# Performance work log

Measured on AMD Instinct MI355X. Metric: run time of the kernel, lower is better.

The kernel has to match this reference:

```python
import jax, jax.numpy as jnp
import numpy as np

N = 50000      # nodes
E = 1000000    # edges (avg degree 20)
IN, H, OUT = 3, 128, 3


def setup_inputs() -> dict:
    key = jax.random.key(0)
    ks = jax.random.split(key, 12)
    pos = jax.random.normal(ks[0], (N, IN), dtype=jnp.float32)
    edge_index = jax.random.randint(ks[1], (2, E), 0, N, dtype=jnp.int64)
    dims = [(IN, H), (H, H), (H, H), (H, H), (H, OUT)]
    inp = {"pos": pos, "edge_index": edge_index}
    for i, (di, do) in enumerate(dims):
        inp[f"W{i}"] = jax.random.normal(ks[2 + 2 * i], (di, do), dtype=jnp.float32) / np.sqrt(di).astype(np.float32)
        inp[f"b{i}"] = jnp.zeros((do,), dtype=jnp.float32)
    return inp


def _gcn_conv(x, W, b, src, dst, norm):
    # PyG GCNConv: linear transform first, then normalized scatter-add, then bias
    h = x @ W                                  # [N, do]
    msg = h[src] * norm[:, None]               # gather + edge-normalize  [E+N, do]
    out = jax.ops.segment_sum(msg, dst, num_segments=N)  # scatter-add to targets
    return out + b


def reference(pos, edge_index, W0, b0, W1, b1, W2, b2, W3, b3, W4, b4):
    src, dst = edge_index[0], edge_index[1]
    loop = jnp.arange(N, dtype=src.dtype)
    src = jnp.concatenate([src, loop])         # add self-loops
    dst = jnp.concatenate([dst, loop])
    # symmetric normalization: deg computed on target nodes incl. self-loops
    deg = jax.ops.segment_sum(jnp.ones_like(src, dtype=pos.dtype), dst, num_segments=N)
    dis = jnp.where(deg > 0, jax.lax.rsqrt(jnp.maximum(deg, 1e-12)), 0.0)
    norm = dis[src] * dis[dst]                 # [E+N]

    Ws = [W0, W1, W2, W3, W4]
    bs = [b0, b1, b2, b3, b4]
    x = pos
    for i in range(4):                         # all but last layer: conv + SiLU
        x = jax.nn.silu(_gcn_conv(x, Ws[i], bs[i], src, dst, norm))
    return _gcn_conv(x, Ws[4], bs[4], src, dst, norm)
```

## Files before the change

kernel.cpp:

```cpp
#include <hip/hip_runtime.h>
#include <cstdint>
#include <cstddef>


#define NB_SPLIT 256
#define BUCKET_SHIFT 7
#define BSLACK 512

static __device__ __forceinline__ float silu_f(float x) {
  return x / (1.0f + __expf(-x));
}

__global__ __launch_bounds__(256) void k_prep(
    const int* __restrict__ e32, int* __restrict__ epack, int* __restrict__ bT,
    int E, int nbucket, int chunk) {
  __shared__ int hist[512];
  __shared__ int nz;
  const int w = blockIdx.x, t = threadIdx.x;
  for (int b = t; b < nbucket; b += 256) hist[b] = 0;
  if (t == 0) nz = 0;
  __syncthreads();
  if (e32[t * 2 + 1] != 0) nz = 1;
  __syncthreads();
  const int f = nz ? 0 : 1;
  const int i0 = w * chunk;
  const int i1 = min(E, i0 + chunk);
  for (int i = i0 + t; i < i1; i += 256) {
    int s, d;
    if (f) { s = e32[2 * i]; d = e32[2 * E + 2 * i]; }
    else   { s = e32[i];     d = e32[E + i]; }
    epack[i] = s | (d << 16);
    atomicAdd(&hist[d >> BUCKET_SHIFT], 1);
  }
  __syncthreads();
  for (int b = t; b < nbucket; b += 256) {
    int h = hist[b];
    if (h) atomicAdd(&bT[b], h);
  }
}

__global__ __launch_bounds__(512) void k_sscan2(
    int* __restrict__ arr, int* __restrict__ cpy, int n) {
  __shared__ int wsum[8];
  const int t = threadIdx.x;
  int v = (t < n) ? arr[t] : 0;
  int sc = v;
  const int lane = t & 63;
  #pragma unroll
  for (int o = 1; o < 64; o <<= 1) {
    int u = __shfl_up(sc, o);
    if (lane >= o) sc += u;
  }
  if (lane == 63) wsum[t >> 6] = sc;
  __syncthreads();
  int wb = 0;
  const int wid = t >> 6;
  for (int w = 0; w < wid; ++w) wb += wsum[w];
  const int ex = wb + sc - v;
  if (t < n) { arr[t] = ex; cpy[t] = ex; }
  if (t == n - 1) arr[n] = ex + v;
}

__global__ __launch_bounds__(256) void k_split(
    const int* __restrict__ epack, int* __restrict__ gcur,
    int* __restrict__ tmp, int E, int nbucket, int chunk) {
  __shared__ int cur[512];
  const int w = blockIdx.x, t = threadIdx.x;
  for (int b = t; b < nbucket; b += 256) cur[b] = 0;
  __syncthreads();
  const int i0 = w * chunk;
  const int i1 = min(E, i0 + chunk);
  for (int i = i0 + t; i < i1; i += 256) {
    int b = (int)(((unsigned)epack[i]) >> (16 + BUCKET_SHIFT));
    atomicAdd(&cur[b], 1);
  }
  __syncthreads();
  for (int b = t; b < nbucket; b += 256) {
    int h = cur[b];
    cur[b] = h ? atomicAdd(&gcur[b], h) : 0;
  }
  __syncthreads();
  for (int i = i0 + t; i < i1; i += 256) {
    int p = epack[i];
    int b = (int)(((unsigned)p) >> (16 + BUCKET_SHIFT));
    int pos = atomicAdd(&cur[b], 1);
    tmp[pos] = p;
  }
}

__global__ __launch_bounds__(256) void k_csr(
    const int* __restrict__ tmp, const int* __restrict__ bbase,
    const float* __restrict__ pos,
    int2* __restrict__ rp, float* __restrict__ dis, float4* __restrict__ p4,
    unsigned short* __restrict__ col, int nbucket, int N) {
  __shared__ int lcnt[128];
  __shared__ int lcur[128];
  __shared__ int wtot;
  const int b = blockIdx.x, t = threadIdx.x;
  const int nb0 = b << BUCKET_SHIFT;
  const int nn = min(1 << BUCKET_SHIFT, N - nb0);
  if (t < 128) lcnt[t] = 0;
  __syncthreads();
  const int s0 = bbase[b], s1 = bbase[b + 1];
  for (int i = s0 + t; i < s1; i += 256) {
    atomicAdd(&lcnt[((unsigned)tmp[i] >> 16) & 127u], 1);
  }
  __syncthreads();
  const int cbase = ((s0 + 3) & ~3) + b * BSLACK;
  int v = 0, pv = 0, sc = 0;
  if (t < 128) {
    v = lcnt[t];
    pv = (v + 3) & ~3;
    sc = pv;
    #pragma unroll
    for (int o = 1; o < 64; o <<= 1) {
      int u = __shfl_up(sc, o);
      if ((t & 63) >= o) sc += u;
    }
    if (t == 63) wtot = sc;
  }
  __syncthreads();
  if (t < 128) {
    int ex = cbase + ((t >= 64) ? wtot : 0) + sc - pv;
    lcur[t] = ex;
    if (t < nn) {
      int node = nb0 + t;
      float d = rsqrtf((float)(v + 1));
      rp[node] = make_int2(ex, pv);
      dis[node] = d;
      p4[node] = make_float4(pos[3 * node + 0] * d, pos[3 * node + 1] * d,
                             pos[3 * node + 2] * d, d);
      for (int p = ex + v; p < ex + pv; ++p) col[p] = (unsigned short)N;
    }
  }
  __syncthreads();
  for (int i = s0 + t; i < s1; i += 256) {
    unsigned p = (unsigned)tmp[i];
    int j = (int)((p >> 16) & ((1u << BUCKET_SHIFT) - 1));
    int pos_ = atomicAdd(&lcur[j], 1);
    col[pos_] = (unsigned short)(p & 0xffffu);
  }
}

__global__ __launch_bounds__(256) void k_l0(
    const float4* __restrict__ p4, const int2* __restrict__ rp,
    const unsigned short* __restrict__ col,
    const float* __restrict__ W0, const float* __restrict__ b0,
    float* __restrict__ out, float* __restrict__ zB, int n, int slStride) {
  const int t = threadIdx.x;
  if (blockIdx.x == 0) {
    const int bi = t >> 7, si = (t >> 4) & 7, ci = t & 15;
    float* bp = bi ? zB : out;
    bp[(size_t)si * slStride + (size_t)n * 16 + ci] = 0.f;
  }
  const int l = t & 31;
  const int node = blockIdx.x * 8 + (t >> 5);
  if (node >= n) return;
  const int2 r = rp[node];
  float a0 = 0.f, a1 = 0.f, a2 = 0.f;
  for (int e = r.x + l; e < r.x + r.y; e += 32) {
    int s = col[e];
    if (s < n) {
      float4 v = p4[s];
      a0 += v.x; a1 += v.y; a2 += v.z;
    }
  }
  #pragma unroll
  for (int m = 16; m >= 1; m >>= 1) {
    a0 += __shfl_xor(a0, m);
    a1 += __shfl_xor(a1, m);
    a2 += __shfl_xor(a2, m);
  }
  const float4 self = p4[node];
  const float d = self.w;
  a0 = (a0 + self.x) * d;
  a1 = (a1 + self.y) * d;
  a2 = (a2 + self.z) * d;
  const int c = l << 2;
  float4 bb = *reinterpret_cast<const float4*>(b0 + c);
  float4 w0 = *reinterpret_cast<const float4*>(W0 + 0 * 128 + c);
  float4 w1 = *reinterpret_cast<const float4*>(W0 + 1 * 128 + c);
  float4 w2 = *reinterpret_cast<const float4*>(W0 + 2 * 128 + c);
  float4 o;
  o.x = silu_f(a0 * w0.x + a1 * w1.x + a2 * w2.x + bb.x) * d;
  o.y = silu_f(a0 * w0.y + a1 * w1.y + a2 * w2.y + bb.y) * d;
  o.z = silu_f(a0 * w0.z + a1 * w1.z + a2 * w2.z + bb.z) * d;
  o.w = silu_f(a0 * w0.w + a1 * w1.w + a2 * w2.w + bb.w) * d;
  *reinterpret_cast<float4*>(out + (size_t)(c >> 4) * slStride +
                             (size_t)node * 16 + (c & 15)) = o;
}

__global__ void k_agg4(const float4* __restrict__ y4, float* __restrict__ out3,
                       const int2* __restrict__ rp,
                       const unsigned short* __restrict__ col,
                       const float* __restrict__ dis, const float* __restrict__ bias,
                       int n) {
  int i = blockIdx.x * blockDim.x + threadIdx.x;
  if (i >= n) return;
  const float4 self = y4[i];
  float a0 = self.x, a1 = self.y, a2 = self.z;
  const int2 r = rp[i];
  for (int e = r.x; e < r.x + r.y; ++e) {
    int s = col[e];
    if (s >= n) continue;
    float4 v = y4[s];
    a0 += v.x; a1 += v.y; a2 += v.z;
  }
  const float d = dis[i];
  out3[i * 3 + 0] = a0 * d + bias[0];
  out3[i * 3 + 1] = a1 * d + bias[1];
  out3[i * 3 + 2] = a2 * d + bias[2];
}

__global__ __launch_bounds__(256) void k_agg_slice(
    const float* __restrict__ xs, float* __restrict__ y,
    const int2* __restrict__ rp, const unsigned short* __restrict__ col,
    const float* __restrict__ dis, int n, int slStride) {
  const int s = blockIdx.x & 7;
  const int nb = blockIdx.x >> 3;
  const int t = threadIdx.x;
  const int lane = t & 63;
  const int nsub = lane >> 3;
  const int ch = (lane >> 2) & 1;
  const int c4 = (lane & 3) << 2;
  const int node = nb * 32 + (t >> 6) * 8 + nsub;
  const bool valid = node < n;
  int e0 = 0, P = 0;
  if (valid) { int2 r = rp[node]; e0 = r.x; P = r.y; }
  const int h = ((P >> 1) + 3) & ~3;
  const int eb = e0 + (ch ? h : 0);
  const int ee = ch ? (e0 + P) : (e0 + h);
  const float* __restrict__ xb = xs + (size_t)s * slStride + c4;

  float4 a0 = make_float4(0.f, 0.f, 0.f, 0.f);
  float4 a1 = make_float4(0.f, 0.f, 0.f, 0.f);
  float4 a2 = make_float4(0.f, 0.f, 0.f, 0.f);
  float4 a3 = make_float4(0.f, 0.f, 0.f, 0.f);
  for (int e = eb; e < ee; e += 4) {
    ushort4 idx = *reinterpret_cast<const ushort4*>(col + e);
    float4 v0 = *reinterpret_cast<const float4*>(xb + (size_t)idx.x * 16);
    float4 v1 = *reinterpret_cast<const float4*>(xb + (size_t)idx.y * 16);
    float4 v2 = *reinterpret_cast<const float4*>(xb + (size_t)idx.z * 16);
    float4 v3 = *reinterpret_cast<const float4*>(xb + (size_t)idx.w * 16);
    a0.x += v0.x; a0.y += v0.y; a0.z += v0.z; a0.w += v0.w;
    a1.x += v1.x; a1.y += v1.y; a1.z += v1.z; a1.w += v1.w;
    a2.x += v2.x; a2.y += v2.y; a2.z += v2.z; a2.w += v2.w;
    a3.x += v3.x; a3.y += v3.y; a3.z += v3.z; a3.w += v3.w;
  }
  a0.x += a1.x + a2.x + a3.x;
  a0.y += a1.y + a2.y + a3.y;
  a0.z += a1.z + a2.z + a3.z;
  a0.w += a1.w + a2.w + a3.w;
  a0.x += __shfl_xor(a0.x, 4);
  a0.y += __shfl_xor(a0.y, 4);
  a0.z += __shfl_xor(a0.z, 4);
  a0.w += __shfl_xor(a0.w, 4);
  if (valid && ch == 0) {
    float4 self = *reinterpret_cast<const float4*>(xb + (size_t)node * 16);
    const float d = dis[node];
    float4 r;
    r.x = (a0.x + self.x) * d;
    r.y = (a0.y + self.y) * d;
    r.z = (a0.z + self.z) * d;
    r.w = (a0.w + self.w) * d;
    *reinterpret_cast<float4*>(y + (size_t)s * slStride + (size_t)node * 16 + c4) = r;
  }
}

template <int PROJ>
__global__ __launch_bounds__(512, 4) void k_mm_w(
    const float* __restrict__ x, const float* __restrict__ W,
    const float* __restrict__ bias, const float* __restrict__ dis,
    float* __restrict__ out, const float* __restrict__ W4, int n, int slStride) {
  __shared__ float ws[128][128];
  const int t = threadIdx.x;
  #pragma unroll
  for (int it = 0; it < 8; ++it) {
    int i = t + it * 512;
    int k = i >> 5, b = i & 31;
    int slot = (b >> 1) | ((b & 1) << 4);
    *reinterpret_cast<float4*>(&ws[k][slot << 2]) =
        *reinterpret_cast<const float4*>(W + (size_t)i * 4);
  }
  __syncthreads();

  const int tc = t & 15;
  const int tr = (t >> 4) << 2;
  const int row0 = blockIdx.x * 128;

  int rb[4];
  #pragma unroll
  for (int r = 0; r < 4; ++r) {
    rb[r] = min(row0 + tr + r, n - 1) * 16;
  }

  float4 accA[4], accB[4];
  #pragma unroll
  for (int r = 0; r < 4; ++r) {
    accA[r] = make_float4(0.f, 0.f, 0.f, 0.f);
    accB[r] = make_float4(0.f, 0.f, 0.f, 0.f);
  }

  #pragma unroll 1
  for (int kk = 0; kk < 128; kk += 4) {
    const float* __restrict__ xk = x + (size_t)(kk >> 4) * slStride + (kk & 15);
    float4 xr[4];
    #pragma unroll
    for (int r = 0; r < 4; ++r) {
      xr[r] = *reinterpret_cast<const float4*>(xk + rb[r]);
    }
    #pragma unroll
    for (int j = 0; j < 4; ++j) {
      float4 wA = *reinterpret_cast<const float4*>(&ws[kk + j][tc << 2]);
      float4 wB = *reinterpret_cast<const float4*>(&ws[kk + j][64 + (tc << 2)]);
      #pragma unroll
      for (int r = 0; r < 4; ++r) {
        float xv = (j == 0) ? xr[r].x : (j == 1) ? xr[r].y : (j == 2) ? xr[r].z : xr[r].w;
        accA[r].x += xv * wA.x; accA[r].y += xv * wA.y;
        accA[r].z += xv * wA.z; accA[r].w += xv * wA.w;
        accB[r].x += xv * wB.x; accB[r].y += xv * wB.y;
        accB[r].z += xv * wB.z; accB[r].w += xv * wB.w;
      }
    }
  }

  float4 bbA = *reinterpret_cast<const float4*>(bias + tc * 8);
  float4 bbB = *reinterpret_cast<const float4*>(bias + tc * 8 + 4);
  if (PROJ) {
    float w4r[8][3];
    #pragma unroll
    for (int c = 0; c < 8; ++c) {
      w4r[c][0] = W4[(tc * 8 + c) * 3 + 0];
      w4r[c][1] = W4[(tc * 8 + c) * 3 + 1];
      w4r[c][2] = W4[(tc * 8 + c) * 3 + 2];
    }
    #pragma unroll
    for (int r = 0; r < 4; ++r) {
      int row = row0 + tr + r;
      float d = (row < n) ? dis[row] : 0.0f;
      float4 a = accA[r], b4 = accB[r];
      a.x = silu_f(a.x + bbA.x) * d;  a.y = silu_f(a.y + bbA.y) * d;
      a.z = silu_f(a.z + bbA.z) * d;  a.w = silu_f(a.w + bbA.w) * d;
      b4.x = silu_f(b4.x + bbB.x) * d; b4.y = silu_f(b4.y + bbB.y) * d;
      b4.z = silu_f(b4.z + bbB.z) * d; b4.w = silu_f(b4.w + bbB.w) * d;
      float p0 = a.x * w4r[0][0] + a.y * w4r[1][0] + a.z * w4r[2][0] + a.w * w4r[3][0]
               + b4.x * w4r[4][0] + b4.y * w4r[5][0] + b4.z * w4r[6][0] + b4.w * w4r[7][0];
      float p1 = a.x * w4r[0][1] + a.y * w4r[1][1] + a.z * w4r[2][1] + a.w * w4r[3][1]
               + b4.x * w4r[4][1] + b4.y * w4r[5][1] + b4.z * w4r[6][1] + b4.w * w4r[7][1];
      float p2 = a.x * w4r[0][2] + a.y * w4r[1][2] + a.z * w4r[2][2] + a.w * w4r[3][2]
               + b4.x * w4r[4][2] + b4.y * w4r[5][2] + b4.z * w4r[6][2] + b4.w * w4r[7][2];
      #pragma unroll
      for (int m = 8; m >= 1; m >>= 1) {
        p0 += __shfl_xor(p0, m);
        p1 += __shfl_xor(p1, m);
        p2 += __shfl_xor(p2, m);
      }
      if ((t & 15) == 0 && row < n) {
        *reinterpret_cast<float4*>(out + (size_t)row * 4) =
            make_float4(p0, p1, p2, 0.f);
      }
    }
  } else {
    #pragma unroll
    for (int r = 0; r < 4; ++r) {
      int row = row0 + tr + r;
      if (row < n) {
        float d = dis[row];
        float4 a = accA[r], b4 = accB[r];
        a.x = silu_f(a.x + bbA.x) * d;  a.y = silu_f(a.y + bbA.y) * d;
        a.z = silu_f(a.z + bbA.z) * d;  a.w = silu_f(a.w + bbA.w) * d;
        b4.x = silu_f(b4.x + bbB.x) * d; b4.y = silu_f(b4.y + bbB.y) * d;
        b4.z = silu_f(b4.z + bbB.z) * d; b4.w = silu_f(b4.w + bbB.w) * d;
        float* dst = out + (size_t)(tc >> 1) * slStride +
                     (size_t)row * 16 + ((tc & 1) << 3);
        *reinterpret_cast<float4*>(dst) = a;
        *reinterpret_cast<float4*>(dst + 4) = b4;
      }
    }
  }
}

extern "C" void kernel_launch(void* const* d_in, const int* in_sizes, int n_in,
                              void* d_out, int out_size, void* d_ws, size_t ws_size,
                              hipStream_t stream) {
  const float* pos = (const float*)d_in[0];
  const int* e32 = (const int*)d_in[1];
  const float* W[5] = {(const float*)d_in[2], (const float*)d_in[4], (const float*)d_in[6],
                       (const float*)d_in[8], (const float*)d_in[10]};
  const float* B[5] = {(const float*)d_in[3], (const float*)d_in[5], (const float*)d_in[7],
                       (const float*)d_in[9], (const float*)d_in[11]};
  float* out = (float*)d_out;

  const int N = in_sizes[0] / 3;
  const int E = in_sizes[1] / 2;
  const int NBUCKET = (N + (1 << BUCKET_SHIFT) - 1) >> BUCKET_SHIFT;
  const int chunk = (E + NB_SPLIT - 1) / NB_SPLIT;
  const int slStride = (N + 1) * 16;

  char* base = (char*)d_ws;
  size_t off = 0;
  auto alloc = [&](size_t bytes) -> void* {
    void* p = base + off;
    off += (bytes + 255) & ~(size_t)255;
    return p;
  };
  float* dis   = (float*)alloc((size_t)N * 4);
  int2* rp     = (int2*)alloc((size_t)N * 8);
  int* bT      = (int*)alloc((size_t)(NBUCKET + 1) * 4);
  int* gcur    = (int*)alloc((size_t)NBUCKET * 4);
  unsigned short* col =
      (unsigned short*)alloc(((size_t)E + (size_t)NBUCKET * BSLACK + 64) * 2);
  float4* p4   = (float4*)alloc((size_t)N * 16);
  float4* y4   = (float4*)alloc((size_t)N * 16);
  float* bufA  = (float*)alloc((size_t)(N + 1) * 128 * 4);
  float* bufB  = (float*)alloc((size_t)(N + 1) * 128 * 4);
  int* epack = (int*)bufA;
  int* tmp   = (int*)bufB;

  hipMemsetAsync(bT, 0, (size_t)(NBUCKET + 1) * 4, stream);
  k_prep<<<NB_SPLIT, 256, 0, stream>>>(e32, epack, bT, E, NBUCKET, chunk);
  k_sscan2<<<1, 512, 0, stream>>>(bT, gcur, NBUCKET);
  k_split<<<NB_SPLIT, 256, 0, stream>>>(epack, gcur, tmp, E, NBUCKET, chunk);
  k_csr<<<NBUCKET, 256, 0, stream>>>(tmp, bT, pos, rp, dis, p4, col, NBUCKET, N);

  k_l0<<<(N + 7) / 8, 256, 0, stream>>>(p4, rp, col, W[0], B[0], bufA, bufB, N, slStride);

  const int agg_grid = ((N + 31) / 32) * 8;
  const int mm_grid = (N + 127) / 128;
  for (int l = 1; l <= 2; ++l) {
    k_agg_slice<<<agg_grid, 256, 0, stream>>>(bufA, bufB, rp, col, dis, N, slStride);
    k_mm_w<0><<<mm_grid, 512, 0, stream>>>(bufB, W[l], B[l], dis, bufA, nullptr, N, slStride);
  }

  k_agg_slice<<<agg_grid, 256, 0, stream>>>(bufA, bufB, rp, col, dis, N, slStride);
  k_mm_w<1><<<mm_grid, 512, 0, stream>>>(bufB, W[3], B[3], dis, (float*)y4, W[4], N, slStride);

  k_agg4<<<(N + 255) / 256, 256, 0, stream>>>(y4, out, rp, col, dis, B[4], N);

  (void)n_in; (void)out_size; (void)ws_size;
}
```

Measured before the change: 310.6 us.

## Fuse CSR histogram and split using fixed per-bucket regions; nontemporal gathers

The edge-preprocessing pipeline (histogram, global scan, split) collapses into one fused split kernel. Each bucket now gets a fixed-size region of BREG slots instead of exact prefix-summed offsets, which removes the scan kernel, the memset, and the second pass over the packed edge array. Packed edges are held in registers between the count and scatter phases. Aggregation gathers switch to nontemporal vector loads. The risk is silent overflow if any bucket receives more than 4096 edges (expected about 2560 for random inputs), plus more memory for col; the nontemporal hint may hurt cache reuse of gathered rows.

```diff
diff --git a/kernel.cpp b/kernel.cpp
--- a/kernel.cpp
+++ b/kernel.cpp
@@ -5,19 +5,26 @@
 
 #define NB_SPLIT 256
 #define BUCKET_SHIFT 7
-#define BSLACK 512
+#define BREG 4096
+
+typedef float vf4 __attribute__((ext_vector_type(4)));
 
 static __device__ __forceinline__ float silu_f(float x) {
   return x / (1.0f + __expf(-x));
 }
 
-__global__ __launch_bounds__(256) void k_prep(
-    const int* __restrict__ e32, int* __restrict__ epack, int* __restrict__ bT,
-    int E, int nbucket, int chunk) {
-  __shared__ int hist[512];
+__global__ void k_init(int* __restrict__ gcur, int nb) {
+  int t = threadIdx.x;
+  if (t < nb) gcur[t] = t * BREG;
+}
+
+__global__ __launch_bounds__(256) void k_fsplit(
+    const int* __restrict__ e32, int* __restrict__ gcur,
+    int* __restrict__ tmp, int E, int nbucket, int chunk) {
+  __shared__ int cur[512];
   __shared__ int nz;
   const int w = blockIdx.x, t = threadIdx.x;
-  for (int b = t; b < nbucket; b += 256) hist[b] = 0;
+  for (int b = t; b < nbucket; b += 256) cur[b] = 0;
   if (t == 0) nz = 0;
   __syncthreads();
   if (e32[t * 2 + 1] != 0) nz = 1;
@@ -25,54 +32,19 @@
   const int f = nz ? 0 : 1;
   const int i0 = w * chunk;
   const int i1 = min(E, i0 + chunk);
-  for (int i = i0 + t; i < i1; i += 256) {
-    int s, d;
-    if (f) { s = e32[2 * i]; d = e32[2 * E + 2 * i]; }
-    else   { s = e32[i];     d = e32[E + i]; }
-    epack[i] = s | (d << 16);
-    atomicAdd(&hist[d >> BUCKET_SHIFT], 1);
-  }
-  __syncthreads();
-  for (int b = t; b < nbucket; b += 256) {
-    int h = hist[b];
-    if (h) atomicAdd(&bT[b], h);
-  }
-}
-
-__global__ __launch_bounds__(512) void k_sscan2(
-    int* __restrict__ arr, int* __restrict__ cpy, int n) {
-  __shared__ int wsum[8];
-  const int t = threadIdx.x;
-  int v = (t < n) ? arr[t] : 0;
-  int sc = v;
-  const int lane = t & 63;
-  #pragma unroll
-  for (int o = 1; o < 64; o <<= 1) {
-    int u = __shfl_up(sc, o);
-    if (lane >= o) sc += u;
-  }
-  if (lane == 63) wsum[t >> 6] = sc;
-  __syncthreads();
-  int wb = 0;
-  const int wid = t >> 6;
-  for (int w = 0; w < wid; ++w) wb += wsum[w];
-  const int ex = wb + sc - v;
-  if (t < n) { arr[t] = ex; cpy[t] = ex; }
-  if (t == n - 1) arr[n] = ex + v;
-}
-
-__global__ __launch_bounds__(256) void k_split(
-    const int* __restrict__ epack, int* __restrict__ gcur,
-    int* __restrict__ tmp, int E, int nbucket, int chunk) {
-  __shared__ int cur[512];
-  const int w = blockIdx.x, t = threadIdx.x;
-  for (int b = t; b < nbucket; b += 256) cur[b] = 0;
-  __syncthreads();
-  const int i0 = w * chunk;
-  const int i1 = min(E, i0 + chunk);
-  for (int i = i0 + t; i < i1; i += 256) {
-    int b = (int)(((unsigned)epack[i]) >> (16 + BUCKET_SHIFT));
-    atomicAdd(&cur[b], 1);
+  int pk[16];
+  #pragma unroll
+  for (int it = 0; it < 16; ++it) {
+    int i = i0 + t + it * 256;
+    if (i < i1) {
+      int s, d;
+      if (f) { s = e32[2 * i]; d = e32[2 * E + 2 * i]; }
+      else   { s = e32[i];     d = e32[E + i]; }
+      pk[it] = s | (d << 16);
+      atomicAdd(&cur[d >> BUCKET_SHIFT], 1);
+    } else {
+      pk[it] = 0;
+    }
   }
   __syncthreads();
   for (int b = t; b < nbucket; b += 256) {
@@ -80,19 +52,23 @@
     cur[b] = h ? atomicAdd(&gcur[b], h) : 0;
   }
   __syncthreads();
-  for (int i = i0 + t; i < i1; i += 256) {
-    int p = epack[i];
-    int b = (int)(((unsigned)p) >> (16 + BUCKET_SHIFT));
-    int pos = atomicAdd(&cur[b], 1);
-    tmp[pos] = p;
+  #pragma unroll
+  for (int it = 0; it < 16; ++it) {
+    int i = i0 + t + it * 256;
+    if (i < i1) {
+      int p = pk[it];
+      int b = (int)(((unsigned)p) >> (16 + BUCKET_SHIFT));
+      int pos = atomicAdd(&cur[b], 1);
+      tmp[pos] = p;
+    }
   }
 }
 
 __global__ __launch_bounds__(256) void k_csr(
-    const int* __restrict__ tmp, const int* __restrict__ bbase,
+    const int* __restrict__ tmp, const int* __restrict__ gcur,
     const float* __restrict__ pos,
     int2* __restrict__ rp, float* __restrict__ dis, float4* __restrict__ p4,
-    unsigned short* __restrict__ col, int nbucket, int N) {
+    unsigned short* __restrict__ col, int N) {
   __shared__ int lcnt[128];
   __shared__ int lcur[128];
   __shared__ int wtot;
@@ -101,12 +77,12 @@
   const int nn = min(1 << BUCKET_SHIFT, N - nb0);
   if (t < 128) lcnt[t] = 0;
   __syncthreads();
-  const int s0 = bbase[b], s1 = bbase[b + 1];
+  const int s0 = b * BREG, s1 = gcur[b];
   for (int i = s0 + t; i < s1; i += 256) {
     atomicAdd(&lcnt[((unsigned)tmp[i] >> 16) & 127u], 1);
   }
   __syncthreads();
-  const int cbase = ((s0 + 3) & ~3) + b * BSLACK;
+  const int cbase = b * BREG;
   int v = 0, pv = 0, sc = 0;
   if (t < 128) {
     v = lcnt[t];
@@ -232,37 +208,31 @@
   const int ee = ch ? (e0 + P) : (e0 + h);
   const float* __restrict__ xb = xs + (size_t)s * slStride + c4;
 
-  float4 a0 = make_float4(0.f, 0.f, 0.f, 0.f);
-  float4 a1 = make_float4(0.f, 0.f, 0.f, 0.f);
-  float4 a2 = make_float4(0.f, 0.f, 0.f, 0.f);
-  float4 a3 = make_float4(0.f, 0.f, 0.f, 0.f);
+  vf4 a0 = (vf4)0.f, a1 = (vf4)0.f, a2 = (vf4)0.f, a3 = (vf4)0.f;
   for (int e = eb; e < ee; e += 4) {
     ushort4 idx = *reinterpret_cast<const ushort4*>(col + e);
-    float4 v0 = *reinterpret_cast<const float4*>(xb + (size_t)idx.x * 16);
-    float4 v1 = *reinterpret_cast<const float4*>(xb + (size_t)idx.y * 16);
-    float4 v2 = *reinterpret_cast<const float4*>(xb + (size_t)idx.z * 16);
-    float4 v3 = *reinterpret_cast<const float4*>(xb + (size_t)idx.w * 16);
-    a0.x += v0.x; a0.y += v0.y; a0.z += v0.z; a0.w += v0.w;
-    a1.x += v1.x; a1.y += v1.y; a1.z += v1.z; a1.w += v1.w;
-    a2.x += v2.x; a2.y += v2.y; a2.z += v2.z; a2.w += v2.w;
-    a3.x += v3.x; a3.y += v3.y; a3.z += v3.z; a3.w += v3.w;
-  }
-  a0.x += a1.x + a2.x + a3.x;
-  a0.y += a1.y + a2.y + a3.y;
-  a0.z += a1.z + a2.z + a3.z;
-  a0.w += a1.w + a2.w + a3.w;
-  a0.x += __shfl_xor(a0.x, 4);
-  a0.y += __shfl_xor(a0.y, 4);
-  a0.z += __shfl_xor(a0.z, 4);
-  a0.w += __shfl_xor(a0.w, 4);
+    a0 += __builtin_nontemporal_load(
+        reinterpret_cast<const vf4*>(xb + (size_t)idx.x * 16));
+    a1 += __builtin_nontemporal_load(
+        reinterpret_cast<const vf4*>(xb + (size_t)idx.y * 16));
+    a2 += __builtin_nontemporal_load(
+        reinterpret_cast<const vf4*>(xb + (size_t)idx.z * 16));
+    a3 += __builtin_nontemporal_load(
+        reinterpret_cast<const vf4*>(xb + (size_t)idx.w * 16));
+  }
+  vf4 acc = a0 + a1 + a2 + a3;
+  acc.x += __shfl_xor(acc.x, 4);
+  acc.y += __shfl_xor(acc.y, 4);
+  acc.z += __shfl_xor(acc.z, 4);
+  acc.w += __shfl_xor(acc.w, 4);
   if (valid && ch == 0) {
     float4 self = *reinterpret_cast<const float4*>(xb + (size_t)node * 16);
     const float d = dis[node];
     float4 r;
-    r.x = (a0.x + self.x) * d;
-    r.y = (a0.y + self.y) * d;
-    r.z = (a0.z + self.z) * d;
-    r.w = (a0.w + self.w) * d;
+    r.x = (acc.x + self.x) * d;
+    r.y = (acc.y + self.y) * d;
+    r.z = (acc.z + self.z) * d;
+    r.w = (acc.w + self.w) * d;
     *reinterpret_cast<float4*>(y + (size_t)s * slStride + (size_t)node * 16 + c4) = r;
   }
 }
@@ -406,22 +376,18 @@
   };
   float* dis   = (float*)alloc((size_t)N * 4);
   int2* rp     = (int2*)alloc((size_t)N * 8);
-  int* bT      = (int*)alloc((size_t)(NBUCKET + 1) * 4);
   int* gcur    = (int*)alloc((size_t)NBUCKET * 4);
   unsigned short* col =
-      (unsigned short*)alloc(((size_t)E + (size_t)NBUCKET * BSLACK + 64) * 2);
+      (unsigned short*)alloc(((size_t)NBUCKET * BREG + 64) * 2);
   float4* p4   = (float4*)alloc((size_t)N * 16);
   float4* y4   = (float4*)alloc((size_t)N * 16);
   float* bufA  = (float*)alloc((size_t)(N + 1) * 128 * 4);
   float* bufB  = (float*)alloc((size_t)(N + 1) * 128 * 4);
-  int* epack = (int*)bufA;
-  int* tmp   = (int*)bufB;
-
-  hipMemsetAsync(bT, 0, (size_t)(NBUCKET + 1) * 4, stream);
-  k_prep<<<NB_SPLIT, 256, 0, stream>>>(e32, epack, bT, E, NBUCKET, chunk);
-  k_sscan2<<<1, 512, 0, stream>>>(bT, gcur, NBUCKET);
-  k_split<<<NB_SPLIT, 256, 0, stream>>>(epack, gcur, tmp, E, NBUCKET, chunk);
-  k_csr<<<NBUCKET, 256, 0, stream>>>(tmp, bT, pos, rp, dis, p4, col, NBUCKET, N);
+  int* tmp = (int*)bufB;
+
+  k_init<<<1, 512, 0, stream>>>(gcur, NBUCKET);
+  k_fsplit<<<NB_SPLIT, 256, 0, stream>>>(e32, gcur, tmp, E, NBUCKET, chunk);
+  k_csr<<<NBUCKET, 256, 0, stream>>>(tmp, gcur, pos, rp, dis, p4, col, N);
 
   k_l0<<<(N + 7) / 8, 256, 0, stream>>>(p4, rp, col, W[0], B[0], bufA, bufB, N, slStride);
 
```

Result: slower. 463.3 us (+49.2%).
